# Kernel tuning notes

Hardware: AMD Instinct MI355X
Metric: run time of the kernel (lower is better)

Reference implementation:

```python
import jax, jax.numpy as jnp
import numpy as np

N = 8192
LATENT_DIM = 64


def setup_inputs() -> dict:
    key = jax.random.key(0)
    kx, ky = jax.random.split(key)
    x = jax.random.normal(kx, (N, LATENT_DIM), dtype=jnp.float32)
    y = jax.random.normal(ky, (N, LATENT_DIM), dtype=jnp.float32)
    return {"x": x, "y": y}


def _rbf_kernel(a, b):
    # Faithful to torch: exp(-mean((a_i - b_j)^2, axis=dim) / dim)
    #                  = exp(-||a_i - b_j||^2 / dim^2)
    # Computed via the expanded-sq-dist identity to avoid the [N, N, dim]
    # tiled intermediate the torch code materializes.
    dim = a.shape[1]
    sq_a = jnp.sum(a * a, axis=1)  # [Na]
    sq_b = jnp.sum(b * b, axis=1)  # [Nb]
    sq_dist = sq_a[:, None] + sq_b[None, :] - 2.0 * (a @ b.T)  # [Na, Nb]
    return jnp.exp(-sq_dist / (dim * dim))


def reference(x, y):
    # MMD with RBF kernel: mean k(x,x) + mean k(y,y) - 2 mean k(x,y)
    kxx = jnp.mean(_rbf_kernel(x, x))
    kyy = jnp.mean(_rbf_kernel(y, y))
    kxy = jnp.mean(_rbf_kernel(x, y))
    return kxx + kyy - 2.0 * kxy
```

## Files before the change

kernel.cpp:

```cpp
#include <hip/hip_runtime.h>
#include <cmath>

#define NPTS 8192
#define DIM 64
#define BT 128

#define LEAF_F   0
#define LEAF_N   (3 * 8192 * 64)
#define ROWS_F   (LEAF_F + LEAF_N)
#define ROWS_N   (3 * 8192)
#define MEANS_F  (ROWS_F + ROWS_N)
#define NX_F     ((MEANS_F + 3 + 3) & ~3)
#define NY_F     (NX_F + 8192)
#define SPLIT_F  (NY_F + 8192)
#define SPLIT_ELEMS (NPTS * DIM)


typedef short bf16x8 __attribute__((ext_vector_type(8)));
typedef float f32x4  __attribute__((ext_vector_type(4)));

__device__ __forceinline__ unsigned short f32_bf16_rne(float f) {
    unsigned u = __float_as_uint(f);
    return (unsigned short)((u + 0x7FFFu + ((u >> 16) & 1u)) >> 16);
}
__device__ __forceinline__ float bf16_f32(unsigned short h) {
    return __uint_as_float(((unsigned)h) << 16);
}

__device__ __forceinline__ float exp2_hw(float x) {
#if __has_builtin(__builtin_amdgcn_exp2f)
    return __builtin_amdgcn_exp2f(x);
#else
    float r;
    asm("v_exp_f32 %0, %1" : "=v"(r) : "v"(x));
    return r;
#endif
}

#define SWZ_XOR1(x)  __int_as_float(__builtin_amdgcn_ds_swizzle(__float_as_int(x), 0x041F))
#define SWZ_XOR2(x)  __int_as_float(__builtin_amdgcn_ds_swizzle(__float_as_int(x), 0x081F))
#define SWZ_XOR4(x)  __int_as_float(__builtin_amdgcn_ds_swizzle(__float_as_int(x), 0x101F))
#define SWZ_XOR8(x)  __int_as_float(__builtin_amdgcn_ds_swizzle(__float_as_int(x), 0x201F))
#define SWZ_XOR16(x) __int_as_float(__builtin_amdgcn_ds_swizzle(__float_as_int(x), 0x401F))

__global__ void prep_kernel(const float* __restrict__ x, const float* __restrict__ y,
                            unsigned short* __restrict__ Xh, unsigned short* __restrict__ Xl,
                            unsigned short* __restrict__ Yh, unsigned short* __restrict__ Yl,
                            float* __restrict__ nx, float* __restrict__ ny) {
    int gtid = blockIdx.x * 256 + threadIdx.x;
    int r  = gtid >> 4;
    int k4 = gtid & 15;
    int isY = r >= NPTS;
    int rr = isY ? r - NPTS : r;
    const float4* Rg = (const float4*)((isY ? y : x) + (size_t)rr * DIM);
    unsigned short* Hh = isY ? Yh : Xh;
    unsigned short* Hl = isY ? Yl : Xl;
    const int t16 = rr >> 4, mrow = rr & 15;
    float4 v = Rg[k4];
    ushort4 h, l;
    h.x = f32_bf16_rne(v.x); l.x = f32_bf16_rne(v.x - bf16_f32(h.x));
    h.y = f32_bf16_rne(v.y); l.y = f32_bf16_rne(v.y - bf16_f32(h.y));
    h.z = f32_bf16_rne(v.z); l.z = f32_bf16_rne(v.z - bf16_f32(h.z));
    h.w = f32_bf16_rne(v.w); l.w = f32_bf16_rne(v.w - bf16_f32(h.w));
    int off = t16 * 1024 + (k4 >> 3) * 512 + ((k4 >> 1) & 3) * 128 + mrow * 8 + (k4 & 1) * 4;
    *(ushort4*)(Hh + off) = h;
    *(ushort4*)(Hl + off) = l;
    float s = v.x * v.x;
    s = fmaf(v.y, v.y, s); s = fmaf(v.z, v.z, s); s = fmaf(v.w, v.w, s);
    s = s + SWZ_XOR1(s);
    s = s + SWZ_XOR2(s);
    s = s + SWZ_XOR4(s);
    s = s + SWZ_XOR8(s);
    if (k4 == 0) { if (isY) ny[rr] = s; else nx[rr] = s; }
}

__global__ __launch_bounds__(512, 3) void mmd_tile_kernel(
    const unsigned short* __restrict__ Xh, const unsigned short* __restrict__ Xl,
    const unsigned short* __restrict__ Yh, const unsigned short* __restrict__ Yl,
    const float* __restrict__ nx, const float* __restrict__ ny,
    float* __restrict__ leafs)
{
    int id  = blockIdx.x + 65 * (blockIdx.y + 64 * blockIdx.z);
    int nid = (id & 7) * 1040 + (id >> 3);
    int zb  = nid >= 4160;
    int rem = nid - zb * 4160;
    int gj  = rem / 65;
    int gi  = rem - gj * 65;

    int zz, bx, by;
    if (zb == 1) {
        if (gi >= 64) return;
        zz = 2; bx = gi; by = gj;
    } else if (gi > gj) {
        zz = 0; by = gj; bx = gi - 1;
    } else {
        zz = 1; by = gi; bx = gj;
    }

    __shared__ float rowpart[2][BT];
    __shared__ float colpart[4][BT];

    const int t = threadIdx.x;
    const size_t arow = (size_t)by * BT;
    const size_t brow = (size_t)bx * BT;
    const int cb = bx;

    const unsigned short* pAh = (zz == 1) ? Yh : Xh;
    const unsigned short* pAl = (zz == 1) ? Yl : Xl;
    const unsigned short* pBh = (zz == 0) ? Xh : Yh;
    const unsigned short* pBl = (zz == 0) ? Xl : Yl;
    const float* nA = (zz == 1) ? ny : nx;
    const float* nB = (zz == 0) ? nx : ny;

    const int lane = t & 63;
    const int wv   = t >> 6;
    const int mrow = lane & 15;
    const int quad = lane >> 4;
    const int rblk = (wv & 3) << 5;
    const int cblk = (wv >> 2) << 6;

    const int aT = by * 8 + (wv & 3) * 2;
    const int bT = bx * 8 + (wv >> 2) * 4;
    const int lsub = quad * 128 + mrow * 8;

    const bool domirror = (zz < 2) && (bx > by);

    float sa[8];
    #pragma unroll
    for (int rt = 0; rt < 2; ++rt)
        #pragma unroll
        for (int i = 0; i < 4; ++i)
            sa[rt * 4 + i] = nA[arow + rblk + rt * 16 + quad * 4 + i];
    float sb[4];
    #pragma unroll
    for (int ct = 0; ct < 4; ++ct)
        sb[ct] = nB[brow + cblk + ct * 16 + mrow];

    bf16x8 fAh[2][2], fAl[2][2];
    #pragma unroll
    for (int rt = 0; rt < 2; ++rt)
        #pragma unroll
        for (int kc = 0; kc < 2; ++kc) {
            int off = (aT + rt) * 1024 + kc * 512 + lsub;
            fAh[rt][kc] = *(const bf16x8*)(pAh + off);
            fAl[rt][kc] = *(const bf16x8*)(pAl + off);
        }

    const float SCL = (float)(-1.4426950408889634 / 4096.0);
    float rs01[2][4] = {{0.f,0.f,0.f,0.f},{0.f,0.f,0.f,0.f}};
    float rs23[2][4] = {{0.f,0.f,0.f,0.f},{0.f,0.f,0.f,0.f}};
    float cs[4];

    const int boff0 = bT * 1024 + lsub;
    bf16x8 cbh0 = *(const bf16x8*)(pBh + boff0);
    bf16x8 cbh1 = *(const bf16x8*)(pBh + boff0 + 512);
    bf16x8 cbl0 = *(const bf16x8*)(pBl + boff0);
    bf16x8 cbl1 = *(const bf16x8*)(pBl + boff0 + 512);

    #pragma unroll
    for (int ct = 0; ct < 4; ++ct) {
        bf16x8 nbh0, nbh1, nbl0, nbl1;
        if (ct < 3) {
            int boff = (bT + ct + 1) * 1024 + lsub;
            nbh0 = *(const bf16x8*)(pBh + boff);
            nbh1 = *(const bf16x8*)(pBh + boff + 512);
            nbl0 = *(const bf16x8*)(pBl + boff);
            nbl1 = *(const bf16x8*)(pBl + boff + 512);
        }

        f32x4 c0 = (f32x4){0.f, 0.f, 0.f, 0.f};
        f32x4 c1 = (f32x4){0.f, 0.f, 0.f, 0.f};
        __builtin_amdgcn_s_setprio(1);
        c0 = __builtin_amdgcn_mfma_f32_16x16x32_bf16(fAh[0][0], cbh0, c0, 0, 0, 0);
        c0 = __builtin_amdgcn_mfma_f32_16x16x32_bf16(fAh[0][0], cbl0, c0, 0, 0, 0);
        c0 = __builtin_amdgcn_mfma_f32_16x16x32_bf16(fAl[0][0], cbh0, c0, 0, 0, 0);
        c0 = __builtin_amdgcn_mfma_f32_16x16x32_bf16(fAh[0][1], cbh1, c0, 0, 0, 0);
        c0 = __builtin_amdgcn_mfma_f32_16x16x32_bf16(fAh[0][1], cbl1, c0, 0, 0, 0);
        c0 = __builtin_amdgcn_mfma_f32_16x16x32_bf16(fAl[0][1], cbh1, c0, 0, 0, 0);
        c1 = __builtin_amdgcn_mfma_f32_16x16x32_bf16(fAh[1][0], cbh0, c1, 0, 0, 0);
        c1 = __builtin_amdgcn_mfma_f32_16x16x32_bf16(fAh[1][0], cbl0, c1, 0, 0, 0);
        c1 = __builtin_amdgcn_mfma_f32_16x16x32_bf16(fAl[1][0], cbh0, c1, 0, 0, 0);
        c1 = __builtin_amdgcn_mfma_f32_16x16x32_bf16(fAh[1][1], cbh1, c1, 0, 0, 0);
        c1 = __builtin_amdgcn_mfma_f32_16x16x32_bf16(fAh[1][1], cbl1, c1, 0, 0, 0);
        c1 = __builtin_amdgcn_mfma_f32_16x16x32_bf16(fAl[1][1], cbh1, c1, 0, 0, 0);
        __builtin_amdgcn_s_setprio(0);

        float k0[4], k1[4];
        #pragma unroll
        for (int i = 0; i < 4; ++i) {
            float d0  = c0[i];
            float s20 = sa[i] + sb[ct];
            k0[i] = exp2_hw((s20 - 2.0f * d0) * SCL);
            float d1  = c1[i];
            float s21 = sa[4 + i] + sb[ct];
            k1[i] = exp2_hw((s21 - 2.0f * d1) * SCL);
        }
        if (ct < 2) {
            #pragma unroll
            for (int i = 0; i < 4; ++i) { rs01[0][i] += k0[i]; rs01[1][i] += k1[i]; }
        } else {
            #pragma unroll
            for (int i = 0; i < 4; ++i) { rs23[0][i] += k0[i]; rs23[1][i] += k1[i]; }
        }
        if (domirror)
            cs[ct] = ((k0[0] + k0[1]) + (k0[2] + k0[3]))
                   + ((k1[0] + k1[1]) + (k1[2] + k1[3]));

        if (ct < 3) {
            cbh0 = nbh0; cbh1 = nbh1; cbl0 = nbl0; cbl1 = nbl1;
        }
    }

    float rs[2][4];
    #pragma unroll
    for (int rt = 0; rt < 2; ++rt)
        #pragma unroll
        for (int i = 0; i < 4; ++i)
            rs[rt][i] = rs01[rt][i] + rs23[rt][i];

    const int b0 = lane & 1;
    const int b1 = (lane >> 1) & 1;
    const int b2 = (lane >> 2) & 1;
    const int b3 = (lane >> 3) & 1;

    float a4[4];
    #pragma unroll
    for (int i = 0; i < 4; ++i) {
        float snd = b3 ? rs[0][i] : rs[1][i];
        float rcv = SWZ_XOR8(snd);
        a4[i] = (b3 ? rs[1][i] : rs[0][i]) + rcv;
    }
    float a2[2];
    #pragma unroll
    for (int j = 0; j < 2; ++j) {
        float snd = b2 ? a4[j] : a4[2 + j];
        float rcv = SWZ_XOR4(snd);
        a2[j] = (b2 ? a4[2 + j] : a4[j]) + rcv;
    }
    {
        float snd = b1 ? a2[0] : a2[1];
        float rcv = SWZ_XOR2(snd);
        float a1  = (b1 ? a2[1] : a2[0]) + rcv;
        float r64 = a1 + SWZ_XOR1(a1);
        if (b0 == 0)
            rowpart[wv >> 2][rblk + b3 * 16 + quad * 4 + b2 * 2 + b1] = r64;
    }

    if (domirror) {
        const int b4 = (lane >> 4) & 1;
        const int b5 = (lane >> 5) & 1;
        float c2[2];
        #pragma unroll
        for (int j = 0; j < 2; ++j) {
            float snd = b4 ? cs[j] : cs[2 + j];
            float rcv = SWZ_XOR16(snd);
            c2[j] = (b4 ? cs[2 + j] : cs[j]) + rcv;
        }
        float snd = b5 ? c2[0] : c2[1];
        float rcv = __shfl_xor(snd, 32);
        float c1v = (b5 ? c2[1] : c2[0]) + rcv;
        colpart[wv & 3][cblk + (b4 * 2 + b5) * 16 + mrow] = c1v;
    }
    __syncthreads();

    if (t < BT) {
        leafs[((size_t)zz * 64 + cb) * 8192 + arow + t] = rowpart[0][t] + rowpart[1][t];
        if (domirror) {
            leafs[((size_t)zz * 64 + by) * 8192 + brow + t] =
                (colpart[0][t] + colpart[1][t]) + (colpart[2][t] + colpart[3][t]);
        }
    }
}

__global__ void rowsum_kernel(const float* __restrict__ leafs, float* __restrict__ rowsums) {
    const int t = threadIdx.x;
    const int wv = t >> 6;
    const int lane = t & 63;
    const int p = lane >> 4;
    const int rlo = lane & 15;
    const int gr = blockIdx.x * 64 + wv * 16 + rlo;
    const int z = gr >> 13;
    const int r = gr & 8191;
    const float* base = leafs + ((size_t)z * 64 + p * 16) * 8192 + r;
    float v[16];
    #pragma unroll
    for (int i = 0; i < 16; ++i) v[i] = base[(size_t)i * 8192];
    #pragma unroll
    for (int n = 8; n >= 1; n >>= 1)
        #pragma unroll
        for (int i = 0; i < 16; ++i)
            if (i < n) v[i] = v[2*i] + v[2*i+1];
    float s = v[0];
    float u = s + SWZ_XOR16(s);
    float w = u + __shfl_xor(u, 32);
    if (p == 0) rowsums[gr] = w;
}

__global__ void colsum_kernel(const float* __restrict__ rowsums, float* __restrict__ out) {
    __shared__ float L[3][256];
    __shared__ float m[3];
    const int t  = threadIdx.x;
    const int z  = t >> 8;
    const int tz = t & 255;
    {
        const float4* src = (const float4*)(rowsums + z * 8192);
        float w[32];
        #pragma unroll
        for (int i = 0; i < 8; ++i) {
            float4 q = src[tz * 8 + i];
            w[4*i+0] = q.x; w[4*i+1] = q.y; w[4*i+2] = q.z; w[4*i+3] = q.w;
        }
        #pragma unroll
        for (int n = 16; n >= 1; n >>= 1)
            #pragma unroll
            for (int i = 0; i < 32; ++i)
                if (i < n) w[i] = w[2*i] + w[2*i+1];
        L[z][tz] = w[0];
    }
    __syncthreads();
    for (int n = 128; n >= 1; n >>= 1) {
        float u = 0.f;
        if (tz < n) u = L[z][2*tz] + L[z][2*tz+1];
        __syncthreads();
        if (tz < n) L[z][tz] = u;
        __syncthreads();
    }
    if (tz == 0) m[z] = L[z][0] * (1.0f / 67108864.0f);
    __syncthreads();
    if (t == 0) {
        float t1 = m[0] + m[1];
        out[0] = t1 - 2.0f * m[2];
    }
}

extern "C" void kernel_launch(void* const* d_in, const int* in_sizes, int n_in,
                              void* d_out, int out_size, void* d_ws, size_t ws_size,
                              hipStream_t stream) {
    const float* x = (const float*)d_in[0];
    const float* y = (const float*)d_in[1];
    float* wsf     = (float*)d_ws;
    float* leafs   = wsf + LEAF_F;
    float* rowsums = wsf + ROWS_F;
    float* nx      = wsf + NX_F;
    float* ny      = wsf + NY_F;
    unsigned short* Xh = (unsigned short*)(wsf + SPLIT_F);
    unsigned short* Xl = Xh + SPLIT_ELEMS;
    unsigned short* Yh = Xl + SPLIT_ELEMS;
    unsigned short* Yl = Yh + SPLIT_ELEMS;

    prep_kernel<<<1024, 256, 0, stream>>>(x, y, Xh, Xl, Yh, Yl, nx, ny);
    dim3 grid(65, 64, 2);
    mmd_tile_kernel<<<grid, 512, 0, stream>>>(Xh, Xl, Yh, Yl, nx, ny, leafs);
    rowsum_kernel<<<384, 256, 0, stream>>>(leafs, rowsums);
    colsum_kernel<<<1, 768, 0, stream>>>(rowsums, (float*)d_out);
}
```

Baseline: 131.1 us.

## Fuse final colsum into rowsum via last-block atomic counter; widen prep stores

```diff
diff --git a/kernel.cpp b/kernel.cpp
--- a/kernel.cpp
+++ b/kernel.cpp
@@ -18,6 +18,7 @@
 
 typedef short bf16x8 __attribute__((ext_vector_type(8)));
 typedef float f32x4  __attribute__((ext_vector_type(4)));
+typedef unsigned short u16x8 __attribute__((ext_vector_type(8)));
 
 __device__ __forceinline__ unsigned short f32_bf16_rne(float f) {
     unsigned u = __float_as_uint(f);
@@ -46,32 +47,41 @@
 __global__ void prep_kernel(const float* __restrict__ x, const float* __restrict__ y,
                             unsigned short* __restrict__ Xh, unsigned short* __restrict__ Xl,
                             unsigned short* __restrict__ Yh, unsigned short* __restrict__ Yl,
-                            float* __restrict__ nx, float* __restrict__ ny) {
+                            float* __restrict__ nx, float* __restrict__ ny,
+                            int* __restrict__ cnt) {
     int gtid = blockIdx.x * 256 + threadIdx.x;
-    int r  = gtid >> 4;
-    int k4 = gtid & 15;
+    if (gtid == 0) cnt[0] = 0;
+    int r = gtid >> 3;
+    int m = gtid & 7;
     int isY = r >= NPTS;
     int rr = isY ? r - NPTS : r;
     const float4* Rg = (const float4*)((isY ? y : x) + (size_t)rr * DIM);
     unsigned short* Hh = isY ? Yh : Xh;
     unsigned short* Hl = isY ? Yl : Xl;
     const int t16 = rr >> 4, mrow = rr & 15;
-    float4 v = Rg[k4];
-    ushort4 h, l;
-    h.x = f32_bf16_rne(v.x); l.x = f32_bf16_rne(v.x - bf16_f32(h.x));
-    h.y = f32_bf16_rne(v.y); l.y = f32_bf16_rne(v.y - bf16_f32(h.y));
-    h.z = f32_bf16_rne(v.z); l.z = f32_bf16_rne(v.z - bf16_f32(h.z));
-    h.w = f32_bf16_rne(v.w); l.w = f32_bf16_rne(v.w - bf16_f32(h.w));
-    int off = t16 * 1024 + (k4 >> 3) * 512 + ((k4 >> 1) & 3) * 128 + mrow * 8 + (k4 & 1) * 4;
-    *(ushort4*)(Hh + off) = h;
-    *(ushort4*)(Hl + off) = l;
-    float s = v.x * v.x;
-    s = fmaf(v.y, v.y, s); s = fmaf(v.z, v.z, s); s = fmaf(v.w, v.w, s);
+    float4 v0 = Rg[2 * m];
+    float4 v1 = Rg[2 * m + 1];
+    u16x8 h, l;
+    h[0] = f32_bf16_rne(v0.x); l[0] = f32_bf16_rne(v0.x - bf16_f32(h[0]));
+    h[1] = f32_bf16_rne(v0.y); l[1] = f32_bf16_rne(v0.y - bf16_f32(h[1]));
+    h[2] = f32_bf16_rne(v0.z); l[2] = f32_bf16_rne(v0.z - bf16_f32(h[2]));
+    h[3] = f32_bf16_rne(v0.w); l[3] = f32_bf16_rne(v0.w - bf16_f32(h[3]));
+    h[4] = f32_bf16_rne(v1.x); l[4] = f32_bf16_rne(v1.x - bf16_f32(h[4]));
+    h[5] = f32_bf16_rne(v1.y); l[5] = f32_bf16_rne(v1.y - bf16_f32(h[5]));
+    h[6] = f32_bf16_rne(v1.z); l[6] = f32_bf16_rne(v1.z - bf16_f32(h[6]));
+    h[7] = f32_bf16_rne(v1.w); l[7] = f32_bf16_rne(v1.w - bf16_f32(h[7]));
+    int off = t16 * 1024 + (m >> 2) * 512 + (m & 3) * 128 + mrow * 8;
+    *(u16x8*)(Hh + off) = h;
+    *(u16x8*)(Hl + off) = l;
+    float s0 = v0.x * v0.x;
+    s0 = fmaf(v0.y, v0.y, s0); s0 = fmaf(v0.z, v0.z, s0); s0 = fmaf(v0.w, v0.w, s0);
+    float s1 = v1.x * v1.x;
+    s1 = fmaf(v1.y, v1.y, s1); s1 = fmaf(v1.z, v1.z, s1); s1 = fmaf(v1.w, v1.w, s1);
+    float s = s0 + s1;
     s = s + SWZ_XOR1(s);
     s = s + SWZ_XOR2(s);
     s = s + SWZ_XOR4(s);
-    s = s + SWZ_XOR8(s);
-    if (k4 == 0) { if (isY) ny[rr] = s; else nx[rr] = s; }
+    if (m == 0) { if (isY) ny[rr] = s; else nx[rr] = s; }
 }
 
 __global__ __launch_bounds__(512, 3) void mmd_tile_kernel(
@@ -272,7 +282,8 @@
     }
 }
 
-__global__ void rowsum_kernel(const float* __restrict__ leafs, float* __restrict__ rowsums) {
+__global__ void redsum_kernel(const float* __restrict__ leafs, float* __restrict__ rowsums,
+                              int* __restrict__ cnt, float* __restrict__ out) {
     const int t = threadIdx.x;
     const int wv = t >> 6;
     const int lane = t & 63;
@@ -294,42 +305,44 @@
     float u = s + SWZ_XOR16(s);
     float w = u + __shfl_xor(u, 32);
     if (p == 0) rowsums[gr] = w;
-}
-
-__global__ void colsum_kernel(const float* __restrict__ rowsums, float* __restrict__ out) {
-    __shared__ float L[3][256];
-    __shared__ float m[3];
-    const int t  = threadIdx.x;
-    const int z  = t >> 8;
-    const int tz = t & 255;
-    {
-        const float4* src = (const float4*)(rowsums + z * 8192);
-        float w[32];
+
+    __threadfence();
+    __shared__ int lastFlag;
+    if (t == 0) lastFlag = (atomicAdd(cnt, 1) == (int)gridDim.x - 1);
+    __syncthreads();
+    if (!lastFlag) return;
+    __threadfence();
+
+    __shared__ float L[256];
+    __shared__ float m3[3];
+    for (int zz = 0; zz < 3; ++zz) {
+        const float4* src = (const float4*)(rowsums + zz * 8192);
+        float w2[32];
         #pragma unroll
         for (int i = 0; i < 8; ++i) {
-            float4 q = src[tz * 8 + i];
-            w[4*i+0] = q.x; w[4*i+1] = q.y; w[4*i+2] = q.z; w[4*i+3] = q.w;
+            float4 q = src[t * 8 + i];
+            w2[4*i+0] = q.x; w2[4*i+1] = q.y; w2[4*i+2] = q.z; w2[4*i+3] = q.w;
         }
         #pragma unroll
         for (int n = 16; n >= 1; n >>= 1)
             #pragma unroll
             for (int i = 0; i < 32; ++i)
-                if (i < n) w[i] = w[2*i] + w[2*i+1];
-        L[z][tz] = w[0];
-    }
-    __syncthreads();
-    for (int n = 128; n >= 1; n >>= 1) {
-        float u = 0.f;
-        if (tz < n) u = L[z][2*tz] + L[z][2*tz+1];
+                if (i < n) w2[i] = w2[2*i] + w2[2*i+1];
+        L[t] = w2[0];
         __syncthreads();
-        if (tz < n) L[z][tz] = u;
+        for (int n = 128; n >= 1; n >>= 1) {
+            float u2 = 0.f;
+            if (t < n) u2 = L[2*t] + L[2*t+1];
+            __syncthreads();
+            if (t < n) L[t] = u2;
+            __syncthreads();
+        }
+        if (t == 0) m3[zz] = L[0] * (1.0f / 67108864.0f);
         __syncthreads();
     }
-    if (tz == 0) m[z] = L[z][0] * (1.0f / 67108864.0f);
-    __syncthreads();
     if (t == 0) {
-        float t1 = m[0] + m[1];
-        out[0] = t1 - 2.0f * m[2];
+        float t1 = m3[0] + m3[1];
+        out[0] = t1 - 2.0f * m3[2];
     }
 }
 
@@ -341,6 +354,7 @@
     float* wsf     = (float*)d_ws;
     float* leafs   = wsf + LEAF_F;
     float* rowsums = wsf + ROWS_F;
+    int*   cnt     = (int*)(wsf + MEANS_F);
     float* nx      = wsf + NX_F;
     float* ny      = wsf + NY_F;
     unsigned short* Xh = (unsigned short*)(wsf + SPLIT_F);
@@ -348,9 +362,8 @@
     unsigned short* Yh = Xl + SPLIT_ELEMS;
     unsigned short* Yl = Yh + SPLIT_ELEMS;
 
-    prep_kernel<<<1024, 256, 0, stream>>>(x, y, Xh, Xl, Yh, Yl, nx, ny);
+    prep_kernel<<<512, 256, 0, stream>>>(x, y, Xh, Xl, Yh, Yl, nx, ny, cnt);
     dim3 grid(65, 64, 2);
     mmd_tile_kernel<<<grid, 512, 0, stream>>>(Xh, Xl, Yh, Yl, nx, ny, leafs);
-    rowsum_kernel<<<384, 256, 0, stream>>>(leafs, rowsums);
-    colsum_kernel<<<1, 768, 0, stream>>>(rowsums, (float*)d_out);
-}
+    redsum_kernel<<<384, 256, 0, stream>>>(leafs, rowsums, cnt, (float*)d_out);
+}
```

Measured after the change: 155.7 us. 1.19x slower.

## Switch tile GEMM to 32x32x16 MFMA and widen prep to 8-element stores

Applied to the files above, without the earlier changes.

```diff
diff --git a/kernel.cpp b/kernel.cpp
--- a/kernel.cpp
+++ b/kernel.cpp
@@ -17,7 +17,8 @@
 
 
 typedef short bf16x8 __attribute__((ext_vector_type(8)));
-typedef float f32x4  __attribute__((ext_vector_type(4)));
+typedef float f32x16 __attribute__((ext_vector_type(16)));
+typedef unsigned short u16x8 __attribute__((ext_vector_type(8)));
 
 __device__ __forceinline__ unsigned short f32_bf16_rne(float f) {
     unsigned u = __float_as_uint(f);
@@ -48,30 +49,37 @@
                             unsigned short* __restrict__ Yh, unsigned short* __restrict__ Yl,
                             float* __restrict__ nx, float* __restrict__ ny) {
     int gtid = blockIdx.x * 256 + threadIdx.x;
-    int r  = gtid >> 4;
-    int k4 = gtid & 15;
+    int r = gtid >> 3;
+    int m = gtid & 7;
     int isY = r >= NPTS;
     int rr = isY ? r - NPTS : r;
     const float4* Rg = (const float4*)((isY ? y : x) + (size_t)rr * DIM);
     unsigned short* Hh = isY ? Yh : Xh;
     unsigned short* Hl = isY ? Yl : Xl;
     const int t16 = rr >> 4, mrow = rr & 15;
-    float4 v = Rg[k4];
-    ushort4 h, l;
-    h.x = f32_bf16_rne(v.x); l.x = f32_bf16_rne(v.x - bf16_f32(h.x));
-    h.y = f32_bf16_rne(v.y); l.y = f32_bf16_rne(v.y - bf16_f32(h.y));
-    h.z = f32_bf16_rne(v.z); l.z = f32_bf16_rne(v.z - bf16_f32(h.z));
-    h.w = f32_bf16_rne(v.w); l.w = f32_bf16_rne(v.w - bf16_f32(h.w));
-    int off = t16 * 1024 + (k4 >> 3) * 512 + ((k4 >> 1) & 3) * 128 + mrow * 8 + (k4 & 1) * 4;
-    *(ushort4*)(Hh + off) = h;
-    *(ushort4*)(Hl + off) = l;
-    float s = v.x * v.x;
-    s = fmaf(v.y, v.y, s); s = fmaf(v.z, v.z, s); s = fmaf(v.w, v.w, s);
+    float4 v0 = Rg[2 * m];
+    float4 v1 = Rg[2 * m + 1];
+    u16x8 h, l;
+    h[0] = f32_bf16_rne(v0.x); l[0] = f32_bf16_rne(v0.x - bf16_f32(h[0]));
+    h[1] = f32_bf16_rne(v0.y); l[1] = f32_bf16_rne(v0.y - bf16_f32(h[1]));
+    h[2] = f32_bf16_rne(v0.z); l[2] = f32_bf16_rne(v0.z - bf16_f32(h[2]));
+    h[3] = f32_bf16_rne(v0.w); l[3] = f32_bf16_rne(v0.w - bf16_f32(h[3]));
+    h[4] = f32_bf16_rne(v1.x); l[4] = f32_bf16_rne(v1.x - bf16_f32(h[4]));
+    h[5] = f32_bf16_rne(v1.y); l[5] = f32_bf16_rne(v1.y - bf16_f32(h[5]));
+    h[6] = f32_bf16_rne(v1.z); l[6] = f32_bf16_rne(v1.z - bf16_f32(h[6]));
+    h[7] = f32_bf16_rne(v1.w); l[7] = f32_bf16_rne(v1.w - bf16_f32(h[7]));
+    int off = t16 * 1024 + (m >> 2) * 512 + (m & 3) * 128 + mrow * 8;
+    *(u16x8*)(Hh + off) = h;
+    *(u16x8*)(Hl + off) = l;
+    float s0 = v0.x * v0.x;
+    s0 = fmaf(v0.y, v0.y, s0); s0 = fmaf(v0.z, v0.z, s0); s0 = fmaf(v0.w, v0.w, s0);
+    float s1 = v1.x * v1.x;
+    s1 = fmaf(v1.y, v1.y, s1); s1 = fmaf(v1.z, v1.z, s1); s1 = fmaf(v1.w, v1.w, s1);
+    float s = s0 + s1;
     s = s + SWZ_XOR1(s);
     s = s + SWZ_XOR2(s);
     s = s + SWZ_XOR4(s);
-    s = s + SWZ_XOR8(s);
-    if (k4 == 0) { if (isY) ny[rr] = s; else nx[rr] = s; }
+    if (m == 0) { if (isY) ny[rr] = s; else nx[rr] = s; }
 }
 
 __global__ __launch_bounds__(512, 3) void mmd_tile_kernel(
@@ -114,152 +122,122 @@
 
     const int lane = t & 63;
     const int wv   = t >> 6;
+    const int wr   = wv & 3;
+    const int wc   = wv >> 2;
+    const int c5   = lane & 31;
+    const int hi   = lane >> 5;
     const int mrow = lane & 15;
-    const int quad = lane >> 4;
-    const int rblk = (wv & 3) << 5;
-    const int cblk = (wv >> 2) << 6;
-
-    const int aT = by * 8 + (wv & 3) * 2;
-    const int bT = bx * 8 + (wv >> 2) * 4;
-    const int lsub = quad * 128 + mrow * 8;
+    const int m16  = c5 >> 4;
 
     const bool domirror = (zz < 2) && (bx > by);
 
-    float sa[8];
-    #pragma unroll
-    for (int rt = 0; rt < 2; ++rt)
-        #pragma unroll
-        for (int i = 0; i < 4; ++i)
-            sa[rt * 4 + i] = nA[arow + rblk + rt * 16 + quad * 4 + i];
-    float sb[4];
-    #pragma unroll
-    for (int ct = 0; ct < 4; ++ct)
-        sb[ct] = nB[brow + cblk + ct * 16 + mrow];
-
-    bf16x8 fAh[2][2], fAl[2][2];
-    #pragma unroll
-    for (int rt = 0; rt < 2; ++rt)
-        #pragma unroll
-        for (int kc = 0; kc < 2; ++kc) {
-            int off = (aT + rt) * 1024 + kc * 512 + lsub;
-            fAh[rt][kc] = *(const bf16x8*)(pAh + off);
-            fAl[rt][kc] = *(const bf16x8*)(pAl + off);
+    float sa[16];
+    #pragma unroll
+    for (int j = 0; j < 16; ++j)
+        sa[j] = nA[arow + wr * 32 + (j & 3) + 8 * (j >> 2) + 4 * hi];
+    float sb0 = nB[brow + wc * 64 + c5];
+    float sb1 = nB[brow + wc * 64 + 32 + c5];
+
+    const int aT = by * 8 + wr * 2 + m16;
+    bf16x8 Ahf[4], Alf[4];
+    #pragma unroll
+    for (int c = 0; c < 4; ++c) {
+        int q8 = c * 2 + hi;
+        int off = aT * 1024 + (q8 >> 2) * 512 + (q8 & 3) * 128 + mrow * 8;
+        Ahf[c] = *(const bf16x8*)(pAh + off);
+        Alf[c] = *(const bf16x8*)(pAl + off);
+    }
+    bf16x8 Bhf[2][4], Blf[2][4];
+    #pragma unroll
+    for (int tt = 0; tt < 2; ++tt) {
+        int bT = bx * 8 + wc * 4 + tt * 2 + m16;
+        #pragma unroll
+        for (int c = 0; c < 4; ++c) {
+            int q8 = c * 2 + hi;
+            int off = bT * 1024 + (q8 >> 2) * 512 + (q8 & 3) * 128 + mrow * 8;
+            Bhf[tt][c] = *(const bf16x8*)(pBh + off);
+            Blf[tt][c] = *(const bf16x8*)(pBl + off);
         }
+    }
+
+    f32x16 acc0 = {0.f,0.f,0.f,0.f,0.f,0.f,0.f,0.f,0.f,0.f,0.f,0.f,0.f,0.f,0.f,0.f};
+    f32x16 acc1 = {0.f,0.f,0.f,0.f,0.f,0.f,0.f,0.f,0.f,0.f,0.f,0.f,0.f,0.f,0.f,0.f};
+
+    __builtin_amdgcn_s_setprio(1);
+    #pragma unroll
+    for (int c = 0; c < 4; ++c) {
+        acc0 = __builtin_amdgcn_mfma_f32_32x32x16_bf16(Ahf[c], Bhf[0][c], acc0, 0, 0, 0);
+        acc1 = __builtin_amdgcn_mfma_f32_32x32x16_bf16(Ahf[c], Bhf[1][c], acc1, 0, 0, 0);
+        acc0 = __builtin_amdgcn_mfma_f32_32x32x16_bf16(Ahf[c], Blf[0][c], acc0, 0, 0, 0);
+        acc1 = __builtin_amdgcn_mfma_f32_32x32x16_bf16(Ahf[c], Blf[1][c], acc1, 0, 0, 0);
+        acc0 = __builtin_amdgcn_mfma_f32_32x32x16_bf16(Alf[c], Bhf[0][c], acc0, 0, 0, 0);
+        acc1 = __builtin_amdgcn_mfma_f32_32x32x16_bf16(Alf[c], Bhf[1][c], acc1, 0, 0, 0);
+    }
+    __builtin_amdgcn_s_setprio(0);
 
     const float SCL = (float)(-1.4426950408889634 / 4096.0);
-    float rs01[2][4] = {{0.f,0.f,0.f,0.f},{0.f,0.f,0.f,0.f}};
-    float rs23[2][4] = {{0.f,0.f,0.f,0.f},{0.f,0.f,0.f,0.f}};
-    float cs[4];
-
-    const int boff0 = bT * 1024 + lsub;
-    bf16x8 cbh0 = *(const bf16x8*)(pBh + boff0);
-    bf16x8 cbh1 = *(const bf16x8*)(pBh + boff0 + 512);
-    bf16x8 cbl0 = *(const bf16x8*)(pBl + boff0);
-    bf16x8 cbl1 = *(const bf16x8*)(pBl + boff0 + 512);
-
-    #pragma unroll
-    for (int ct = 0; ct < 4; ++ct) {
-        bf16x8 nbh0, nbh1, nbl0, nbl1;
-        if (ct < 3) {
-            int boff = (bT + ct + 1) * 1024 + lsub;
-            nbh0 = *(const bf16x8*)(pBh + boff);
-            nbh1 = *(const bf16x8*)(pBh + boff + 512);
-            nbl0 = *(const bf16x8*)(pBl + boff);
-            nbl1 = *(const bf16x8*)(pBl + boff + 512);
-        }
-
-        f32x4 c0 = (f32x4){0.f, 0.f, 0.f, 0.f};
-        f32x4 c1 = (f32x4){0.f, 0.f, 0.f, 0.f};
-        __builtin_amdgcn_s_setprio(1);
-        c0 = __builtin_amdgcn_mfma_f32_16x16x32_bf16(fAh[0][0], cbh0, c0, 0, 0, 0);
-        c0 = __builtin_amdgcn_mfma_f32_16x16x32_bf16(fAh[0][0], cbl0, c0, 0, 0, 0);
-        c0 = __builtin_amdgcn_mfma_f32_16x16x32_bf16(fAl[0][0], cbh0, c0, 0, 0, 0);
-        c0 = __builtin_amdgcn_mfma_f32_16x16x32_bf16(fAh[0][1], cbh1, c0, 0, 0, 0);
-        c0 = __builtin_amdgcn_mfma_f32_16x16x32_bf16(fAh[0][1], cbl1, c0, 0, 0, 0);
-        c0 = __builtin_amdgcn_mfma_f32_16x16x32_bf16(fAl[0][1], cbh1, c0, 0, 0, 0);
-        c1 = __builtin_amdgcn_mfma_f32_16x16x32_bf16(fAh[1][0], cbh0, c1, 0, 0, 0);
-        c1 = __builtin_amdgcn_mfma_f32_16x16x32_bf16(fAh[1][0], cbl0, c1, 0, 0, 0);
-        c1 = __builtin_amdgcn_mfma_f32_16x16x32_bf16(fAl[1][0], cbh0, c1, 0, 0, 0);
-        c1 = __builtin_amdgcn_mfma_f32_16x16x32_bf16(fAh[1][1], cbh1, c1, 0, 0, 0);
-        c1 = __builtin_amdgcn_mfma_f32_16x16x32_bf16(fAh[1][1], cbl1, c1, 0, 0, 0);
-        c1 = __builtin_amdgcn_mfma_f32_16x16x32_bf16(fAl[1][1], cbh1, c1, 0, 0, 0);
-        __builtin_amdgcn_s_setprio(0);
-
-        float k0[4], k1[4];
-        #pragma unroll
-        for (int i = 0; i < 4; ++i) {
-            float d0  = c0[i];
-            float s20 = sa[i] + sb[ct];
-            k0[i] = exp2_hw((s20 - 2.0f * d0) * SCL);
-            float d1  = c1[i];
-            float s21 = sa[4 + i] + sb[ct];
-            k1[i] = exp2_hw((s21 - 2.0f * d1) * SCL);
-        }
-        if (ct < 2) {
-            #pragma unroll
-            for (int i = 0; i < 4; ++i) { rs01[0][i] += k0[i]; rs01[1][i] += k1[i]; }
-        } else {
-            #pragma unroll
-            for (int i = 0; i < 4; ++i) { rs23[0][i] += k0[i]; rs23[1][i] += k1[i]; }
-        }
-        if (domirror)
-            cs[ct] = ((k0[0] + k0[1]) + (k0[2] + k0[3]))
-                   + ((k1[0] + k1[1]) + (k1[2] + k1[3]));
-
-        if (ct < 3) {
-            cbh0 = nbh0; cbh1 = nbh1; cbl0 = nbl0; cbl1 = nbl1;
-        }
-    }
-
-    float rs[2][4];
-    #pragma unroll
-    for (int rt = 0; rt < 2; ++rt)
-        #pragma unroll
-        for (int i = 0; i < 4; ++i)
-            rs[rt][i] = rs01[rt][i] + rs23[rt][i];
+    float k0[16], k1[16];
+    #pragma unroll
+    for (int j = 0; j < 16; ++j) {
+        k0[j] = exp2_hw((sa[j] + sb0 - 2.0f * acc0[j]) * SCL);
+        k1[j] = exp2_hw((sa[j] + sb1 - 2.0f * acc1[j]) * SCL);
+    }
+
+    float rsv[16];
+    #pragma unroll
+    for (int j = 0; j < 16; ++j) rsv[j] = k0[j] + k1[j];
 
     const int b0 = lane & 1;
     const int b1 = (lane >> 1) & 1;
     const int b2 = (lane >> 2) & 1;
     const int b3 = (lane >> 3) & 1;
-
+    const int b4 = (lane >> 4) & 1;
+
+    float a8[8];
+    #pragma unroll
+    for (int i = 0; i < 8; ++i) {
+        float snd = b0 ? rsv[i] : rsv[i + 8];
+        float rcv = SWZ_XOR1(snd);
+        a8[i] = (b0 ? rsv[i + 8] : rsv[i]) + rcv;
+    }
     float a4[4];
     #pragma unroll
     for (int i = 0; i < 4; ++i) {
-        float snd = b3 ? rs[0][i] : rs[1][i];
+        float snd = b1 ? a8[i] : a8[i + 4];
+        float rcv = SWZ_XOR2(snd);
+        a4[i] = (b1 ? a8[i + 4] : a8[i]) + rcv;
+    }
+    float a2[2];
+    #pragma unroll
+    for (int i = 0; i < 2; ++i) {
+        float snd = b2 ? a4[i] : a4[i + 2];
+        float rcv = SWZ_XOR4(snd);
+        a2[i] = (b2 ? a4[i + 2] : a4[i]) + rcv;
+    }
+    {
+        float snd = b3 ? a2[0] : a2[1];
         float rcv = SWZ_XOR8(snd);
-        a4[i] = (b3 ? rs[1][i] : rs[0][i]) + rcv;
-    }
-    float a2[2];
-    #pragma unroll
-    for (int j = 0; j < 2; ++j) {
-        float snd = b2 ? a4[j] : a4[2 + j];
-        float rcv = SWZ_XOR4(snd);
-        a2[j] = (b2 ? a4[2 + j] : a4[j]) + rcv;
-    }
-    {
-        float snd = b1 ? a2[0] : a2[1];
-        float rcv = SWZ_XOR2(snd);
-        float a1  = (b1 ? a2[1] : a2[0]) + rcv;
-        float r64 = a1 + SWZ_XOR1(a1);
-        if (b0 == 0)
-            rowpart[wv >> 2][rblk + b3 * 16 + quad * 4 + b2 * 2 + b1] = r64;
+        float a1  = (b3 ? a2[1] : a2[0]) + rcv;
+        float r64 = a1 + SWZ_XOR16(a1);
+        if (b4 == 0)
+            rowpart[wc][wr * 32 + 16 * b0 + 8 * b1 + 2 * b2 + b3 + 4 * hi] = r64;
     }
 
     if (domirror) {
-        const int b4 = (lane >> 4) & 1;
-        const int b5 = (lane >> 5) & 1;
-        float c2[2];
-        #pragma unroll
-        for (int j = 0; j < 2; ++j) {
-            float snd = b4 ? cs[j] : cs[2 + j];
-            float rcv = SWZ_XOR16(snd);
-            c2[j] = (b4 ? cs[2 + j] : cs[j]) + rcv;
+        float w0[16], w1[16];
+        #pragma unroll
+        for (int j = 0; j < 16; ++j) { w0[j] = k0[j]; w1[j] = k1[j]; }
+        #pragma unroll
+        for (int n = 8; n >= 1; n >>= 1)
+            #pragma unroll
+            for (int i = 0; i < 16; ++i)
+                if (i < n) { w0[i] = w0[2*i] + w0[2*i+1]; w1[i] = w1[2*i] + w1[2*i+1]; }
+        float f0 = w0[0] + __shfl_xor(w0[0], 32);
+        float f1 = w1[0] + __shfl_xor(w1[0], 32);
+        if (hi == 0) {
+            colpart[wr][wc * 64 + c5]      = f0;
+            colpart[wr][wc * 64 + 32 + c5] = f1;
         }
-        float snd = b5 ? c2[0] : c2[1];
-        float rcv = __shfl_xor(snd, 32);
-        float c1v = (b5 ? c2[1] : c2[0]) + rcv;
-        colpart[wv & 3][cblk + (b4 * 2 + b5) * 16 + mrow] = c1v;
     }
     __syncthreads();
 
@@ -348,7 +326,7 @@
     unsigned short* Yh = Xl + SPLIT_ELEMS;
     unsigned short* Yl = Yh + SPLIT_ELEMS;
 
-    prep_kernel<<<1024, 256, 0, stream>>>(x, y, Xh, Xl, Yh, Yl, nx, ny);
+    prep_kernel<<<512, 256, 0, stream>>>(x, y, Xh, Xl, Yh, Yl, nx, ny);
     dim3 grid(65, 64, 2);
     mmd_tile_kernel<<<grid, 512, 0, stream>>>(Xh, Xl, Yh, Yl, nx, ny, leafs);
     rowsum_kernel<<<384, 256, 0, stream>>>(leafs, rowsums);
```

Result: slower. 173.6 us (+32.4%).
